# Optimization experiments

Measured on AMD Instinct MI355X. Metric: run time of the kernel, lower is better.

Reference implementation:

```python
import jax, jax.numpy as jnp
import numpy as np

NUM_HEADS = 16
DIM = 2048
SEQ = 2048
ROPE_BASE = 10000.0
EPS = 1.1920929e-07  # torch.finfo(float32).eps, F.rms_norm default


def rms_norm(x):
    return x * jax.lax.rsqrt(jnp.mean(x * x, axis=-1, keepdims=True) + EPS)


def rotary(x):
    # x: [B, T, H, Dh]; rotate halves with per-position freqs
    B, T, H, Dh = x.shape
    inv_freq = (1.0 / ROPE_BASE) ** (jnp.arange(0, Dh, 2, dtype=jnp.float32) / Dh)
    freqs = jnp.arange(T, dtype=jnp.float32)[:, None] * inv_freq[None, :]  # [T, Dh/2]
    cos = jnp.cos(freqs)[None, :, None, :]
    sin = jnp.sin(freqs)[None, :, None, :]
    x1, x2 = jnp.split(x, 2, axis=-1)
    y1 = x1 * cos + x2 * sin
    y2 = -x1 * sin + x2 * cos
    return jnp.concatenate([y1, y2], axis=-1).astype(x.dtype)


def setup_inputs() -> dict:
    key = jax.random.key(0)
    ks = jax.random.split(key, 7)
    s = 1.0 / np.sqrt(DIM)
    return {
        "x": jax.random.normal(ks[0], (1, SEQ, DIM), dtype=jnp.float32),
        "vi": jax.random.normal(ks[1], (1, SEQ, DIM), dtype=jnp.float32),
        "wq": jax.random.normal(ks[2], (DIM, DIM), dtype=jnp.float32) * s,
        "wk": jax.random.normal(ks[3], (DIM, DIM), dtype=jnp.float32) * s,
        "wv": jax.random.normal(ks[4], (DIM, DIM), dtype=jnp.float32) * s,
        "wproj": jax.random.normal(ks[5], (DIM, DIM), dtype=jnp.float32) * s,
        "lambdas": jax.random.uniform(ks[6], (2,), dtype=jnp.float32),
    }


def reference(x, vi, wq, wk, wv, wproj, lambdas):
    B, T, D = x.shape
    H = NUM_HEADS
    Dh = D // H
    # CastedLinear: F.linear(x, W) == x @ W.T, no bias
    q = (x @ wq.T).reshape(B, T, H, Dh)
    k = (x @ wk.T).reshape(B, T, H, Dh)
    v = (x @ wv.T).reshape(B, T, H, Dh)
    v = lambdas[0] * v + lambdas[1] * vi.reshape(B, T, H, Dh)
    q, k = rms_norm(q), rms_norm(k)
    q, k = rotary(q), rotary(k)
    # causal attention (block_mask in source is causal), scale = 1/sqrt(Dh)
    scores = jnp.einsum("bthd,bshd->bhts", q, k) / jnp.sqrt(jnp.float32(Dh))
    causal = jnp.tril(jnp.ones((T, T), dtype=bool))
    scores = jnp.where(causal[None, None, :, :], scores, jnp.float32(-1e30))
    attn = jax.nn.softmax(scores, axis=-1)
    y = jnp.einsum("bhts,bshd->bthd", attn, v).reshape(B, T, D)
    return y @ wproj.T
```

## Files before the change

### kernel.cpp

```cpp
#include <hip/hip_runtime.h>

#define TSEQ 2048
#define DM   2048
#define NHEAD 16

typedef __bf16 bf16x8 __attribute__((ext_vector_type(8)));
typedef float  f32x4  __attribute__((ext_vector_type(4)));
typedef unsigned short ushort8v __attribute__((ext_vector_type(8)));
typedef unsigned int u32x4v __attribute__((ext_vector_type(4)));
typedef const __attribute__((address_space(1))) void* gas_cvp;
typedef __attribute__((address_space(3))) void* las_vp;

__device__ __forceinline__ unsigned short f2bf(float f) {
  unsigned int u = __builtin_bit_cast(unsigned int, f);
  u += 0x7FFFu + ((u >> 16) & 1u);
  return (unsigned short)(u >> 16);
}

__global__ __launch_bounds__(256) void cvt5(const float* __restrict__ x,
                                            const float* __restrict__ wq,
                                            const float* __restrict__ wk,
                                            const float* __restrict__ wv,
                                            const float* __restrict__ wp,
                                            unsigned short* __restrict__ xb,
                                            unsigned short* __restrict__ wqkvb,
                                            unsigned short* __restrict__ wpb) {
  const int NEL = DM * TSEQ;
  int gid = blockIdx.x * 256 + threadIdx.x;
  int seg = gid >> 19;
  int i = gid & ((1 << 19) - 1);
  const float* src;
  unsigned short* dst;
  switch (seg) {
    case 0: src = x;  dst = xb;                      break;
    case 1: src = wq; dst = wqkvb;                   break;
    case 2: src = wk; dst = wqkvb + (size_t)NEL;     break;
    case 3: src = wv; dst = wqkvb + (size_t)2 * NEL; break;
    default: src = wp; dst = wpb;                    break;
  }
  const float4* p = (const float4*)src + (size_t)i * 2;
  float4 a = p[0], b = p[1];
  ushort8v o;
  o[0] = f2bf(a.x); o[1] = f2bf(a.y); o[2] = f2bf(a.z); o[3] = f2bf(a.w);
  o[4] = f2bf(b.x); o[5] = f2bf(b.y); o[6] = f2bf(b.z); o[7] = f2bf(b.w);
  *((ushort8v*)dst + i) = o;
}

__global__ __launch_bounds__(512, 2) void gemm_qkv(const unsigned short* __restrict__ A,
                                                   const unsigned short* __restrict__ B,
                                                   float* __restrict__ C) {
  constexpr int TB = (256 + 192) * 128;
  __shared__ char lds[2 * TB];

  int orig = blockIdx.x;
  int swz = (orig & 7) * 32 + (orig >> 3);
  int bx = swz & 31, by = swz >> 5;
  int tileM = by * 256, tileN = bx * 192;

  int tid = threadIdx.x, w = tid >> 6, lane = tid & 63;
  int l15 = lane & 15, l4 = lane >> 4;
  int wm = w >> 1, wn = w & 1;
  int xorsw = (l15 & 7) << 4;
  int srow = tid >> 3, scolb = (tid & 7) * 16;

  const char* Ag = (const char*)A;
  const char* Bg = (const char*)B;

  f32x4 acc[4][6] = {};

  auto stage = [&](int kt, int bsel) {
    char* dst0 = lds + bsel * TB + srow * 128 + scolb;
    #pragma unroll
    for (int i = 0; i < 7; ++i) {
      int row = i * 64 + srow;
      const char* src = (row < 256 ? Ag + (size_t)(tileM + row) * 4096
                                   : Bg + (size_t)(tileN + row - 256) * 4096)
                        + kt * 128 + (scolb ^ ((row & 7) << 4));
      __builtin_amdgcn_global_load_lds((gas_cvp)src, (las_vp)(dst0 + i * 8192), 16, 0, 0);
    }
  };

  stage(0, 0);
  #pragma unroll 2
  for (int t = 0; t < 32; ++t) {
    int buf = t & 1;
    asm volatile("s_waitcnt vmcnt(0)" ::: "memory");
    __builtin_amdgcn_s_barrier();
    asm volatile("" ::: "memory");
    if (t + 1 < 32) stage(t + 1, buf ^ 1);
    __builtin_amdgcn_sched_barrier(0);

    const char* Lb = lds + buf * TB;
    bf16x8 a[4][2], b[6][2];
    #pragma unroll
    for (int mf = 0; mf < 4; ++mf)
      #pragma unroll
      for (int kk = 0; kk < 2; ++kk)
        a[mf][kk] = *(const bf16x8*)(Lb + (wm * 64 + mf * 16 + l15) * 128 + ((kk * 64 + l4 * 16) ^ xorsw));
    #pragma unroll
    for (int nf = 0; nf < 6; ++nf)
      #pragma unroll
      for (int kk = 0; kk < 2; ++kk)
        b[nf][kk] = *(const bf16x8*)(Lb + 32768 + (wn * 96 + nf * 16 + l15) * 128 + ((kk * 64 + l4 * 16) ^ xorsw));
    #pragma unroll
    for (int kk = 0; kk < 2; ++kk)
      #pragma unroll
      for (int mf = 0; mf < 4; ++mf)
        #pragma unroll
        for (int nf = 0; nf < 6; ++nf)
          acc[mf][nf] = __builtin_amdgcn_mfma_f32_16x16x32_bf16(a[mf][kk], b[nf][kk], acc[mf][nf], 0, 0, 0);
  }

  #pragma unroll
  for (int mf = 0; mf < 4; ++mf) {
    int r0 = tileM + wm * 64 + mf * 16 + l4 * 4;
    #pragma unroll
    for (int nf = 0; nf < 6; ++nf) {
      int c0 = tileN + wn * 96 + nf * 16 + l15;
      #pragma unroll
      for (int j = 0; j < 4; ++j)
        C[(size_t)(r0 + j) * 6144 + c0] = acc[mf][nf][j];
    }
  }
}

__global__ __launch_bounds__(512, 2) void gemm_proj(const unsigned short* __restrict__ A,
                                                    const unsigned short* __restrict__ B,
                                                    float* __restrict__ C) {
  constexpr int TB = 256 * 128;
  __shared__ char lds[3 * TB];

  int orig = blockIdx.x;
  int swz = (orig & 7) * 32 + (orig >> 3);
  int bx = swz & 15, by = swz >> 4;
  int tileM = by * 128, tileN = bx * 128;

  int tid = threadIdx.x, w = tid >> 6, lane = tid & 63;
  int l15 = lane & 15, l4 = lane >> 4;
  int wm = w >> 2, wn = (w >> 1) & 1, ks = w & 1;
  int xorsw = (l15 & 7) << 4;
  int srow = tid >> 3, scolb = (tid & 7) * 16;
  int kb = ks * 64;

  const char* Ag = (const char*)A;
  const char* Bg = (const char*)B;

  f32x4 acc[4][4] = {};

  auto stage = [&](int kt, int bsel) {
    char* dst0 = lds + bsel * TB + srow * 128 + scolb;
    #pragma unroll
    for (int i = 0; i < 4; ++i) {
      int row = i * 64 + srow;
      const char* src = (row < 128 ? Ag + (size_t)(tileM + row) * 4096
                                   : Bg + (size_t)(tileN + row - 128) * 4096)
                        + kt * 128 + (scolb ^ ((row & 7) << 4));
      __builtin_amdgcn_global_load_lds((gas_cvp)src, (las_vp)(dst0 + i * 8192), 16, 0, 0);
    }
  };

  stage(0, 0);
  stage(1, 1);
  #pragma unroll 3
  for (int t = 0; t < 32; ++t) {
    int buf = t % 3;
    if (t + 1 < 32) { asm volatile("s_waitcnt vmcnt(4)" ::: "memory"); }
    else            { asm volatile("s_waitcnt vmcnt(0)" ::: "memory"); }
    __builtin_amdgcn_s_barrier();
    __builtin_amdgcn_sched_barrier(0);
    if (t + 2 < 32) stage(t + 2, (t + 2) % 3);

    const char* Lb = lds + buf * TB;
    bf16x8 a[4], b[4];
    #pragma unroll
    for (int mf = 0; mf < 4; ++mf)
      a[mf] = *(const bf16x8*)(Lb + (wm * 64 + mf * 16 + l15) * 128 + ((kb + l4 * 16) ^ xorsw));
    #pragma unroll
    for (int nf = 0; nf < 4; ++nf)
      b[nf] = *(const bf16x8*)(Lb + (128 + wn * 64 + nf * 16 + l15) * 128 + ((kb + l4 * 16) ^ xorsw));
    #pragma unroll
    for (int mf = 0; mf < 4; ++mf)
      #pragma unroll
      for (int nf = 0; nf < 4; ++nf)
        acc[mf][nf] = __builtin_amdgcn_mfma_f32_16x16x32_bf16(a[mf], b[nf], acc[mf][nf], 0, 0, 0);
  }

  __syncthreads();
  int pair = w >> 1;
  if (ks == 1) {
    #pragma unroll
    for (int mf = 0; mf < 4; ++mf)
      #pragma unroll
      for (int nf = 0; nf < 4; ++nf)
        *(f32x4*)(lds + pair * 16384 + ((mf * 4 + nf) * 64 + lane) * 16) = acc[mf][nf];
  }
  __syncthreads();
  if (ks == 0) {
    #pragma unroll
    for (int mf = 0; mf < 4; ++mf) {
      int r0 = tileM + wm * 64 + mf * 16 + l4 * 4;
      #pragma unroll
      for (int nf = 0; nf < 4; ++nf) {
        f32x4 o = acc[mf][nf] + *(const f32x4*)(lds + pair * 16384 + ((mf * 4 + nf) * 64 + lane) * 16);
        int c0 = tileN + wn * 64 + nf * 16 + l15;
        #pragma unroll
        for (int j = 0; j < 4; ++j)
          C[(size_t)(r0 + j) * 2048 + c0] = o[j];
      }
    }
  }
}

__global__ __launch_bounds__(256) void qkv_post(const float* __restrict__ qkv,
                                                const float* __restrict__ vi,
                                                const float* __restrict__ lam,
                                                unsigned short* __restrict__ qb,
                                                unsigned short* __restrict__ kb,
                                                unsigned short* __restrict__ vb) {
  int wid = blockIdx.x * 4 + (threadIdx.x >> 6);
  int lane = threadIdx.x & 63;
  int t = wid >> 4, h = wid & 15;
  const float* base = qkv + (size_t)t * (3 * DM) + h * 128;
  float l0 = lam[0], l1 = lam[1];

  float invf = exp2f((float)lane * -0.20762050593046014f);
  float ang = (float)t * invf;
  float sn, cs;
  sincosf(ang, &sn, &cs);

  size_t ob = (size_t)t * DM + h * 128;
  {
    float a = base[lane], b = base[lane + 64];
    float ss = a * a + b * b;
    #pragma unroll
    for (int m = 1; m < 64; m <<= 1) ss += __shfl_xor(ss, m, 64);
    float sc = rsqrtf(ss * (1.0f / 128.0f) + 1.1920929e-07f);
    a *= sc; b *= sc;
    qb[ob + lane]      = f2bf(a * cs + b * sn);
    qb[ob + 64 + lane] = f2bf(b * cs - a * sn);
  }
  {
    float a = base[2048 + lane], b = base[2048 + 64 + lane];
    float ss = a * a + b * b;
    #pragma unroll
    for (int m = 1; m < 64; m <<= 1) ss += __shfl_xor(ss, m, 64);
    float sc = rsqrtf(ss * (1.0f / 128.0f) + 1.1920929e-07f);
    a *= sc; b *= sc;
    kb[ob + lane]      = f2bf(a * cs + b * sn);
    kb[ob + 64 + lane] = f2bf(b * cs - a * sn);
  }
  {
    const float* vib = vi + (size_t)t * DM + h * 128;
    vb[ob + lane]      = f2bf(l0 * base[4096 + lane]      + l1 * vib[lane]);
    vb[ob + 64 + lane] = f2bf(l0 * base[4096 + 64 + lane] + l1 * vib[lane + 64]);
  }
}

__global__ __launch_bounds__(256) void transpose_v(const unsigned short* __restrict__ vb,
                                                   unsigned short* __restrict__ vbT) {
  __shared__ __align__(16) unsigned short tile[64][68];
  int t0 = blockIdx.x * 64, d0 = blockIdx.y * 64, h = blockIdx.z;
  int tid = threadIdx.x;
  int li = tid >> 4;
  int lj = (tid & 15) * 4;
  #pragma unroll
  for (int p = 0; p < 4; ++p) {
    int i = p * 16 + li;
    ushort4 v = *(const ushort4*)(vb + (size_t)(t0 + i) * DM + h * 128 + d0 + lj);
    tile[i][lj] = v.x; tile[i][lj + 1] = v.y; tile[i][lj + 2] = v.z; tile[i][lj + 3] = v.w;
  }
  __syncthreads();
  #pragma unroll
  for (int p = 0; p < 4; ++p) {
    int j = p * 16 + li;
    ushort4 wv;
    wv.x = tile[lj][j]; wv.y = tile[lj + 1][j]; wv.z = tile[lj + 2][j]; wv.w = tile[lj + 3][j];
    *(ushort4*)(vbT + (size_t)h * 128 * TSEQ + (size_t)(d0 + j) * TSEQ + t0 + lj) = wv;
  }
}

__global__ __launch_bounds__(256, 2) void attn_split(const unsigned short* __restrict__ qb,
                                                     const unsigned short* __restrict__ kb,
                                                     const unsigned short* __restrict__ vbT,
                                                     float* __restrict__ Opart,
                                                     float2* __restrict__ ml) {
  __shared__ __align__(16) char Ks[2][16384];
  __shared__ __align__(16) char Vs[2][16384];

  int bi = blockIdx.x;
  int qblk = 15 - (bi >> 5);
  int h = (bi >> 1) & 15;
  int s = bi & 1;
  int half = qblk + 1;
  int st0 = s ? half : 0;
  int st1 = s ? 2 * half : half;

  int tid = threadIdx.x, w = tid >> 6, lane = tid & 63;
  int l15 = lane & 15, l4 = lane >> 4;
  int qr0 = qblk * 128 + w * 32;
  int xorK = (l15 & 7) << 4;
  int srcA = ((((l4 << 1)) & 3) * 16 + l15) << 2;
  int srcB = ((((l4 << 1) + 1) & 3) * 16 + l15) << 2;
  bool hi4 = (l4 >> 1) != 0;

  bf16x8 q_frag[2][4];
  #pragma unroll
  for (int qt = 0; qt < 2; ++qt) {
    const unsigned short* qrow = qb + (size_t)(qr0 + qt * 16 + l15) * DM + h * 128 + l4 * 8;
    #pragma unroll
    for (int kk = 0; kk < 4; ++kk) q_frag[qt][kk] = *(const bf16x8*)(qrow + kk * 32);
  }

  const char* kbase = (const char*)kb + (size_t)h * 256;
  const char* vbase = (const char*)vbT + (size_t)h * 128 * TSEQ * 2;

  f32x4 acc_o[2][8] = {};
  float mrow[2] = {-1e30f, -1e30f};
  float lrow[2] = {0.f, 0.f};
  const float scale = 0.08838834764831845f;

  auto stage = [&](int st, int bsel) {
    const char* kb1 = kbase + (size_t)st * 64 * 4096;
    const char* vb1 = vbase + (size_t)st * 64 * 2;
    #pragma unroll
    for (int it = 0; it < 4; ++it) {
      int L = (it * 256 + tid) * 16;
      int row = L >> 8, b = L & 255;
      const char* src = kb1 + (size_t)row * 4096 + (b ^ ((row & 7) << 4));
      __builtin_amdgcn_global_load_lds((gas_cvp)src, (las_vp)(&Ks[bsel][0] + L), 16, 0, 0);
    }
    #pragma unroll
    for (int it = 0; it < 4; ++it) {
      int L = (it * 256 + tid) * 16;
      int row = L >> 7, b = L & 127;
      const char* src = vb1 + (size_t)row * (TSEQ * 2) + (b ^ ((row & 7) << 4));
      __builtin_amdgcn_global_load_lds((gas_cvp)src, (las_vp)(&Vs[bsel][0] + L), 16, 0, 0);
    }
  };

  stage(st0, 0);
  int buf = 0;

  for (int st = st0; st < st1; ++st) {
    asm volatile("s_waitcnt vmcnt(0) lgkmcnt(0)" ::: "memory");
    __builtin_amdgcn_s_barrier();
    __builtin_amdgcn_sched_barrier(0);
    if (st + 1 < st1) stage(st + 1, buf ^ 1);

    f32x4 acc_s[2][4] = {};
    __builtin_amdgcn_s_setprio(1);
    #pragma unroll
    for (int j = 0; j < 4; ++j) {
      const char* kr = &Ks[buf][0] + (j * 16 + l15) * 256;
      #pragma unroll
      for (int kk = 0; kk < 4; ++kk) {
        bf16x8 kf = *(const bf16x8*)(kr + ((l4 * 16 + kk * 64) ^ xorK));
        acc_s[0][j] = __builtin_amdgcn_mfma_f32_16x16x32_bf16(kf, q_frag[0][kk], acc_s[0][j], 0, 0, 0);
        acc_s[1][j] = __builtin_amdgcn_mfma_f32_16x16x32_bf16(kf, q_frag[1][kk], acc_s[1][j], 0, 0, 0);
      }
    }
    __builtin_amdgcn_s_setprio(0);

    int kv0 = st * 64;
    bool needmask = (kv0 + 63) > qr0;
    u32x4v pf[2][2];

    #pragma unroll
    for (int qt = 0; qt < 2; ++qt) {
      int qg = qr0 + qt * 16 + l15;
      float sv[4][4];
      float pmax = -1e30f;
      if (needmask) {
        #pragma unroll
        for (int j = 0; j < 4; ++j)
          #pragma unroll
          for (int r = 0; r < 4; ++r) {
            float v = acc_s[qt][j][r] * scale;
            if ((kv0 + j * 16 + l4 * 4 + r) > qg) v = -1e30f;
            sv[j][r] = v;
            pmax = fmaxf(pmax, v);
          }
      } else {
        #pragma unroll
        for (int j = 0; j < 4; ++j)
          #pragma unroll
          for (int r = 0; r < 4; ++r) {
            float v = acc_s[qt][j][r] * scale;
            sv[j][r] = v;
            pmax = fmaxf(pmax, v);
          }
      }
      pmax = fmaxf(pmax, __shfl_xor(pmax, 16, 64));
      pmax = fmaxf(pmax, __shfl_xor(pmax, 32, 64));
      float mn = fmaxf(mrow[qt], pmax);
      float f = __expf(mrow[qt] - mn);
      mrow[qt] = mn;

      float psum = 0.f;
      unsigned pk[4][2];
      #pragma unroll
      for (int j = 0; j < 4; ++j)
        #pragma unroll
        for (int rr = 0; rr < 2; ++rr) {
          float p0 = __expf(sv[j][2 * rr] - mn);
          float p1 = __expf(sv[j][2 * rr + 1] - mn);
          psum += p0 + p1;
          pk[j][rr] = (unsigned)f2bf(p0) | ((unsigned)f2bf(p1) << 16);
        }
      psum += __shfl_xor(psum, 16, 64);
      psum += __shfl_xor(psum, 32, 64);
      lrow[qt] = lrow[qt] * f + psum;
      #pragma unroll
      for (int n = 0; n < 8; ++n) acc_o[qt][n] *= f;

      #pragma unroll
      for (int kk = 0; kk < 2; ++kk) {
        u32x4v pw;
        #pragma unroll
        for (int w2 = 0; w2 < 4; ++w2) {
          int rr = w2 & 1;
          int src = (w2 < 2) ? srcA : srcB;
          unsigned c0 = (unsigned)__builtin_amdgcn_ds_bpermute(src, (int)pk[2 * kk][rr]);
          unsigned c1 = (unsigned)__builtin_amdgcn_ds_bpermute(src, (int)pk[2 * kk + 1][rr]);
          pw[w2] = hi4 ? c1 : c0;
        }
        pf[qt][kk] = pw;
      }
    }

    __builtin_amdgcn_s_setprio(1);
    #pragma unroll
    for (int kk = 0; kk < 2; ++kk) {
      bf16x8 pb0 = __builtin_bit_cast(bf16x8, pf[0][kk]);
      bf16x8 pb1 = __builtin_bit_cast(bf16x8, pf[1][kk]);
      #pragma unroll
      for (int n = 0; n < 8; ++n) {
        bf16x8 vf = *(const bf16x8*)(&Vs[buf][0] + (n * 16 + l15) * 128 + ((kk * 64 + l4 * 16) ^ xorK));
        acc_o[0][n] = __builtin_amdgcn_mfma_f32_16x16x32_bf16(vf, pb0, acc_o[0][n], 0, 0, 0);
        acc_o[1][n] = __builtin_amdgcn_mfma_f32_16x16x32_bf16(vf, pb1, acc_o[1][n], 0, 0, 0);
      }
    }
    __builtin_amdgcn_s_setprio(0);
    buf ^= 1;
  }

  float* Op = Opart + (size_t)s * (TSEQ * DM);
  #pragma unroll
  for (int qt = 0; qt < 2; ++qt) {
    int q = qr0 + qt * 16 + l15;
    #pragma unroll
    for (int n = 0; n < 8; ++n)
      *(f32x4*)(Op + (size_t)q * DM + h * 128 + n * 16 + l4 * 4) = acc_o[qt][n];
    if (l4 == 0)
      ml[(size_t)s * (TSEQ * NHEAD) + (size_t)q * NHEAD + h] = make_float2(mrow[qt], lrow[qt]);
  }
}

__global__ __launch_bounds__(256) void attn_combine(const float* __restrict__ Opart,
                                                    const float2* __restrict__ ml,
                                                    unsigned short* __restrict__ yb) {
  int idx = blockIdx.x * 256 + threadIdx.x;
  int rowid = idx >> 5;
  float2 ml0 = ml[rowid];
  float2 ml1 = ml[TSEQ * NHEAD + rowid];
  float m = fmaxf(ml0.x, ml1.x);
  float a0 = __expf(ml0.x - m), a1 = __expf(ml1.x - m);
  float inv = 1.0f / (a0 * ml0.y + a1 * ml1.y);
  float4 o0 = ((const float4*)Opart)[idx];
  float4 o1 = ((const float4*)(Opart + (size_t)TSEQ * DM))[idx];
  ushort4 r;
  r.x = f2bf((a0 * o0.x + a1 * o1.x) * inv);
  r.y = f2bf((a0 * o0.y + a1 * o1.y) * inv);
  r.z = f2bf((a0 * o0.z + a1 * o1.z) * inv);
  r.w = f2bf((a0 * o0.w + a1 * o1.w) * inv);
  *(ushort4*)(yb + (size_t)idx * 4) = r;
}

extern "C" void kernel_launch(void* const* d_in, const int* in_sizes, int n_in,
                              void* d_out, int out_size, void* d_ws, size_t ws_size,
                              hipStream_t stream) {
  const float* x   = (const float*)d_in[0];
  const float* vi  = (const float*)d_in[1];
  const float* wq  = (const float*)d_in[2];
  const float* wk  = (const float*)d_in[3];
  const float* wv  = (const float*)d_in[4];
  const float* wp  = (const float*)d_in[5];
  const float* lam = (const float*)d_in[6];

  const size_t MB = 1024 * 1024;
  const int NEL = DM * TSEQ;
  const int N8  = NEL / 8;
  char* ws = (char*)d_ws;
  unsigned short* xb    = (unsigned short*)(ws);
  unsigned short* wqkvb = (unsigned short*)(ws + 8  * MB);
  unsigned short* wpb   = (unsigned short*)(ws + 32 * MB);
  float*          qkv32 = (float*)(ws + 40 * MB);
  float*          Opart = (float*)(ws + 40 * MB);
  float2*         mlbuf = (float2*)(ws + 72 * MB);
  unsigned short* qb2   = (unsigned short*)(ws + 88 * MB);
  unsigned short* kb2   = (unsigned short*)(ws + 96 * MB);
  unsigned short* vb    = (unsigned short*)(ws + 104 * MB);
  unsigned short* vbT   = (unsigned short*)(ws + 112 * MB);
  unsigned short* yb    = (unsigned short*)(ws + 120 * MB);

  cvt5<<<5 * N8 / 256, 256, 0, stream>>>(x, wq, wk, wv, wp, xb, wqkvb, wpb);

  gemm_qkv<<<256, 512, 0, stream>>>(xb, wqkvb, qkv32);

  qkv_post<<<(TSEQ * NHEAD) / 4, 256, 0, stream>>>(qkv32, vi, lam, qb2, kb2, vb);

  transpose_v<<<dim3(TSEQ / 64, 2, NHEAD), 256, 0, stream>>>(vb, vbT);

  attn_split<<<512, 256, 0, stream>>>(qb2, kb2, vbT, Opart, mlbuf);
  attn_combine<<<(TSEQ * DM / 4) / 256, 256, 0, stream>>>(Opart, mlbuf, yb);

  gemm_proj<<<256, 512, 0, stream>>>(yb, wpb, (float*)d_out);
}
```

Before: 174.2 us.

## Split attention KV four ways with 256-row blocks and lazy softmax rescale

Result: no change. 171.9 us (median of 4 runs) (-1.4%).

```diff
diff --git a/kernel.cpp b/kernel.cpp
--- a/kernel.cpp
+++ b/kernel.cpp
@@ -279,25 +279,25 @@
   }
 }
 
-__global__ __launch_bounds__(256, 2) void attn_split(const unsigned short* __restrict__ qb,
+__global__ __launch_bounds__(512, 2) void attn_split(const unsigned short* __restrict__ qb,
                                                      const unsigned short* __restrict__ kb,
                                                      const unsigned short* __restrict__ vbT,
-                                                     float* __restrict__ Opart,
+                                                     float* __restrict__ O01,
+                                                     float* __restrict__ O23,
                                                      float2* __restrict__ ml) {
   __shared__ __align__(16) char Ks[2][16384];
   __shared__ __align__(16) char Vs[2][16384];
 
   int bi = blockIdx.x;
-  int qblk = 15 - (bi >> 5);
-  int h = (bi >> 1) & 15;
-  int s = bi & 1;
-  int half = qblk + 1;
-  int st0 = s ? half : 0;
-  int st1 = s ? 2 * half : half;
+  int qblk = 7 - (bi >> 6);
+  int h = (bi >> 2) & 15;
+  int s = bi & 3;
+  int len = qblk + 1;
+  int st0 = s * len, st1 = st0 + len;
 
   int tid = threadIdx.x, w = tid >> 6, lane = tid & 63;
   int l15 = lane & 15, l4 = lane >> 4;
-  int qr0 = qblk * 128 + w * 32;
+  int qr0 = qblk * 256 + w * 32;
   int xorK = (l15 & 7) << 4;
   int srcA = ((((l4 << 1)) & 3) * 16 + l15) << 2;
   int srcB = ((((l4 << 1) + 1) & 3) * 16 + l15) << 2;
@@ -323,15 +323,15 @@
     const char* kb1 = kbase + (size_t)st * 64 * 4096;
     const char* vb1 = vbase + (size_t)st * 64 * 2;
     #pragma unroll
-    for (int it = 0; it < 4; ++it) {
-      int L = (it * 256 + tid) * 16;
+    for (int it = 0; it < 2; ++it) {
+      int L = (it * 512 + tid) * 16;
       int row = L >> 8, b = L & 255;
       const char* src = kb1 + (size_t)row * 4096 + (b ^ ((row & 7) << 4));
       __builtin_amdgcn_global_load_lds((gas_cvp)src, (las_vp)(&Ks[bsel][0] + L), 16, 0, 0);
     }
     #pragma unroll
-    for (int it = 0; it < 4; ++it) {
-      int L = (it * 256 + tid) * 16;
+    for (int it = 0; it < 2; ++it) {
+      int L = (it * 512 + tid) * 16;
       int row = L >> 7, b = L & 127;
       const char* src = vb1 + (size_t)row * (TSEQ * 2) + (b ^ ((row & 7) << 4));
       __builtin_amdgcn_global_load_lds((gas_cvp)src, (las_vp)(&Vs[bsel][0] + L), 16, 0, 0);
@@ -392,9 +392,16 @@
       }
       pmax = fmaxf(pmax, __shfl_xor(pmax, 16, 64));
       pmax = fmaxf(pmax, __shfl_xor(pmax, 32, 64));
-      float mn = fmaxf(mrow[qt], pmax);
-      float f = __expf(mrow[qt] - mn);
-      mrow[qt] = mn;
+
+      if (!__all(pmax - mrow[qt] <= 8.0f)) {
+        float mn = fmaxf(mrow[qt], pmax);
+        float f = __expf(mrow[qt] - mn);
+        mrow[qt] = mn;
+        lrow[qt] *= f;
+        #pragma unroll
+        for (int n = 0; n < 8; ++n) acc_o[qt][n] *= f;
+      }
+      float mn = mrow[qt];
 
       float psum = 0.f;
       unsigned pk[4][2];
@@ -405,13 +412,13 @@
           float p0 = __expf(sv[j][2 * rr] - mn);
           float p1 = __expf(sv[j][2 * rr + 1] - mn);
           psum += p0 + p1;
-          pk[j][rr] = (unsigned)f2bf(p0) | ((unsigned)f2bf(p1) << 16);
+          unsigned pkw;
+          asm("v_cvt_pk_bf16_f32 %0, %1, %2" : "=v"(pkw) : "v"(p0), "v"(p1));
+          pk[j][rr] = pkw;
         }
       psum += __shfl_xor(psum, 16, 64);
       psum += __shfl_xor(psum, 32, 64);
-      lrow[qt] = lrow[qt] * f + psum;
-      #pragma unroll
-      for (int n = 0; n < 8; ++n) acc_o[qt][n] *= f;
+      lrow[qt] += psum;
 
       #pragma unroll
       for (int kk = 0; kk < 2; ++kk) {
@@ -444,7 +451,8 @@
     buf ^= 1;
   }
 
-  float* Op = Opart + (size_t)s * (TSEQ * DM);
+  float* Op = (s < 2 ? O01 + (size_t)s * (TSEQ * DM)
+                     : O23 + (size_t)(s - 2) * (TSEQ * DM));
   #pragma unroll
   for (int qt = 0; qt < 2; ++qt) {
     int q = qr0 + qt * 16 + l15;
@@ -456,23 +464,30 @@
   }
 }
 
-__global__ __launch_bounds__(256) void attn_combine(const float* __restrict__ Opart,
+__global__ __launch_bounds__(256) void attn_combine(const float* __restrict__ O01,
+                                                    const float* __restrict__ O23,
                                                     const float2* __restrict__ ml,
                                                     unsigned short* __restrict__ yb) {
+  const int TN = TSEQ * NHEAD;
   int idx = blockIdx.x * 256 + threadIdx.x;
   int rowid = idx >> 5;
-  float2 ml0 = ml[rowid];
-  float2 ml1 = ml[TSEQ * NHEAD + rowid];
-  float m = fmaxf(ml0.x, ml1.x);
-  float a0 = __expf(ml0.x - m), a1 = __expf(ml1.x - m);
-  float inv = 1.0f / (a0 * ml0.y + a1 * ml1.y);
-  float4 o0 = ((const float4*)Opart)[idx];
-  float4 o1 = ((const float4*)(Opart + (size_t)TSEQ * DM))[idx];
+  float2 m0 = ml[rowid];
+  float2 m1 = ml[TN + rowid];
+  float2 m2 = ml[2 * TN + rowid];
+  float2 m3 = ml[3 * TN + rowid];
+  float m = fmaxf(fmaxf(m0.x, m1.x), fmaxf(m2.x, m3.x));
+  float a0 = __expf(m0.x - m), a1 = __expf(m1.x - m);
+  float a2 = __expf(m2.x - m), a3 = __expf(m3.x - m);
+  float inv = 1.0f / (a0 * m0.y + a1 * m1.y + a2 * m2.y + a3 * m3.y);
+  float4 o0 = ((const float4*)O01)[idx];
+  float4 o1 = ((const float4*)(O01 + (size_t)TSEQ * DM))[idx];
+  float4 o2 = ((const float4*)O23)[idx];
+  float4 o3 = ((const float4*)(O23 + (size_t)TSEQ * DM))[idx];
   ushort4 r;
-  r.x = f2bf((a0 * o0.x + a1 * o1.x) * inv);
-  r.y = f2bf((a0 * o0.y + a1 * o1.y) * inv);
-  r.z = f2bf((a0 * o0.z + a1 * o1.z) * inv);
-  r.w = f2bf((a0 * o0.w + a1 * o1.w) * inv);
+  r.x = f2bf((a0 * o0.x + a1 * o1.x + a2 * o2.x + a3 * o3.x) * inv);
+  r.y = f2bf((a0 * o0.y + a1 * o1.y + a2 * o2.y + a3 * o3.y) * inv);
+  r.z = f2bf((a0 * o0.z + a1 * o1.z + a2 * o2.z + a3 * o3.z) * inv);
+  r.w = f2bf((a0 * o0.w + a1 * o1.w + a2 * o2.w + a3 * o3.w) * inv);
   *(ushort4*)(yb + (size_t)idx * 4) = r;
 }
 
@@ -495,7 +510,8 @@
   unsigned short* wqkvb = (unsigned short*)(ws + 8  * MB);
   unsigned short* wpb   = (unsigned short*)(ws + 32 * MB);
   float*          qkv32 = (float*)(ws + 40 * MB);
-  float*          Opart = (float*)(ws + 40 * MB);
+  float*          O01   = (float*)(ws);
+  float*          O23   = (float*)(ws + 40 * MB);
   float2*         mlbuf = (float2*)(ws + 72 * MB);
   unsigned short* qb2   = (unsigned short*)(ws + 88 * MB);
   unsigned short* kb2   = (unsigned short*)(ws + 96 * MB);
@@ -511,8 +527,8 @@
 
   transpose_v<<<dim3(TSEQ / 64, 2, NHEAD), 256, 0, stream>>>(vb, vbT);
 
-  attn_split<<<512, 256, 0, stream>>>(qb2, kb2, vbT, Opart, mlbuf);
-  attn_combine<<<(TSEQ * DM / 4) / 256, 256, 0, stream>>>(Opart, mlbuf, yb);
+  attn_split<<<512, 512, 0, stream>>>(qb2, kb2, vbT, O01, O23, mlbuf);
+  attn_combine<<<(TSEQ * DM / 4) / 256, 256, 0, stream>>>(O01, O23, mlbuf, yb);
 
   gemm_proj<<<256, 512, 0, stream>>>(yb, wpb, (float*)d_out);
 }
```
